# Kernel optimization log

Hardware: AMD Instinct MI355X
Metric: run time of the kernel (lower is better)

## Reference

```python
import jax, jax.numpy as jnp
import numpy as np
import math

BS, QLEN, DIM, NHEADS = 2, 2048, 1024, 16
DPH = DIM // NHEADS


def setup_inputs() -> dict:
    key = jax.random.key(0)
    ks = jax.random.split(key, 10)
    s = 0.02
    return {
        "input": jax.random.normal(ks[0], (BS, QLEN, DIM), jnp.float32),
        "mask": jax.random.randint(ks[1], (BS, QLEN), 0, 2, jnp.int32),
        "Wq": jax.random.normal(ks[2], (DIM, DIM), jnp.float32) * s,
        "bq": jnp.zeros((DIM,), jnp.float32),
        "Wk": jax.random.normal(ks[3], (DIM, DIM), jnp.float32) * s,
        "bk": jnp.zeros((DIM,), jnp.float32),
        "Wv": jax.random.normal(ks[4], (DIM, DIM), jnp.float32) * s,
        "bv": jnp.zeros((DIM,), jnp.float32),
        "Wo": jax.random.normal(ks[5], (DIM, DIM), jnp.float32) * s,
        "bo": jnp.zeros((DIM,), jnp.float32),
    }


def _shape(x):
    # (bs, len, dim) -> (bs, heads, len, dph)
    return x.reshape(BS, -1, NHEADS, DPH).transpose(0, 2, 1, 3)


def reference(input, mask, Wq, bq, Wk, bk, Wv, bv, Wo, bo):
    q = _shape(input @ Wq.T + bq)
    k = _shape(input @ Wk.T + bk)
    v = _shape(input @ Wv.T + bv)
    q = q / math.sqrt(DPH)
    scores = jnp.einsum("bhqd,bhkd->bhqk", q, k)  # (bs, h, qlen, klen)
    # original masked_fill_ with 1e-10 (NOT -inf)
    m = (mask == 0)[:, None, None, :]  # (bs,1,1,klen)
    scores = jnp.where(m, jnp.float32(1e-10), scores)
    weights = jax.nn.softmax(scores.astype(jnp.float32), axis=-1).astype(scores.dtype)
    # dropout p=0.0 / eval mode -> identity
    context = jnp.einsum("bhqk,bhkd->bhqd", weights, v)
    context = context.transpose(0, 2, 1, 3).reshape(BS, -1, DIM)
    return context @ Wo.T + bo
```

## Files before the change

kernel.cpp:

```cpp
#include <hip/hip_runtime.h>

typedef __attribute__((ext_vector_type(8))) _Float16 half8;
typedef __attribute__((ext_vector_type(4))) _Float16 half4;
typedef __attribute__((ext_vector_type(4))) float f32x4;
typedef __attribute__((ext_vector_type(16))) float f32x16;
typedef __attribute__((ext_vector_type(4))) int int4v;

#define BS 2
#define QLEN 2048
#define DIM 1024
#define NH 16
#define DPH 64
#define MTOT (BS * QLEN)
#define LOG2E 1.44269504088896340736f

__global__ void cvt_f32_f16(const float* __restrict__ src,
                            _Float16* __restrict__ dst, int n4) {
    int i = blockIdx.x * blockDim.x + threadIdx.x;
    int stride = gridDim.x * blockDim.x;
    for (int idx = i; idx < n4; idx += stride) {
        float4 v = ((const float4*)src)[idx];
        half4 o;
        o[0] = (_Float16)v.x; o[1] = (_Float16)v.y;
        o[2] = (_Float16)v.z; o[3] = (_Float16)v.w;
        ((half4*)dst)[idx] = o;
    }
}

__global__ void cvt_w4(const float* __restrict__ w0, const float* __restrict__ w1,
                       const float* __restrict__ w2, const float* __restrict__ w3,
                       _Float16* __restrict__ d0, _Float16* __restrict__ d1,
                       _Float16* __restrict__ d2, _Float16* __restrict__ d3) {
    const float* src = (blockIdx.y == 0) ? w0 : (blockIdx.y == 1) ? w1
                     : (blockIdx.y == 2) ? w2 : w3;
    _Float16* dst = (blockIdx.y == 0) ? d0 : (blockIdx.y == 1) ? d1
                  : (blockIdx.y == 2) ? d2 : d3;
    int idx = blockIdx.x * blockDim.x + threadIdx.x;
    float4 v = ((const float4*)src)[idx];
    half4 o;
    o[0] = (_Float16)v.x; o[1] = (_Float16)v.y;
    o[2] = (_Float16)v.z; o[3] = (_Float16)v.w;
    ((half4*)dst)[idx] = o;
}

__device__ __forceinline__ void gload_lds16(const _Float16* g, _Float16* l) {
    __builtin_amdgcn_global_load_lds(
        (const __attribute__((address_space(1))) void*)g,
        (__attribute__((address_space(3))) void*)l, 16, 0, 0);
}

__global__ __launch_bounds__(256) void gemm_qkv(
    const _Float16* __restrict__ A,
    const _Float16* __restrict__ Wq, const _Float16* __restrict__ Wk,
    const _Float16* __restrict__ Wv,
    const float* __restrict__ bq, const float* __restrict__ bk,
    const float* __restrict__ bv, const int* __restrict__ mask,
    _Float16* __restrict__ Qd, _Float16* __restrict__ Kd,
    _Float16* __restrict__ Vd) {
    const int K = 1024;
    __shared__ _Float16 sA[2][128 * 32];
    __shared__ _Float16 sB[2][128 * 32];
    const int z = blockIdx.z;
    const _Float16* W = (z == 0) ? Wq : (z == 1) ? Wk : Wv;
    const float* bias = (z == 0) ? bq : (z == 1) ? bk : bv;
    const int m0 = blockIdx.y * 128, n0 = blockIdx.x * 128;
    const int tid = threadIdx.x, w = tid >> 6, l = tid & 63;
    const int wr = (w >> 1) * 64, wc = (w & 1) * 64;
    const int r = l & 15, g = l >> 4;

    auto stage = [&](int k0, int bb) {
#pragma unroll
        for (int i = 0; i < 2; ++i) {
            int c = tid + i * 256;
            int row = c >> 2, seg = (c & 3) * 8;
            gload_lds16(&A[(size_t)(m0 + row) * K + k0 + seg], &sA[bb][c * 8]);
            gload_lds16(&W[(size_t)(n0 + row) * K + k0 + seg], &sB[bb][c * 8]);
        }
    };

    f32x4 acc[4][4] = {};

    stage(0, 0);
    __syncthreads();
    int buf = 0;
    for (int k0 = 0; k0 < K; k0 += 32) {
        if (k0 + 32 < K) stage(k0 + 32, buf ^ 1);

        half8 af[4], bf[4];
#pragma unroll
        for (int i = 0; i < 4; ++i) {
            af[i] = *(const half8*)&sA[buf][(wr + i * 16 + r) * 32 + g * 8];
            bf[i] = *(const half8*)&sB[buf][(wc + i * 16 + r) * 32 + g * 8];
        }
#pragma unroll
        for (int i = 0; i < 4; ++i)
#pragma unroll
            for (int j = 0; j < 4; ++j)
                acc[i][j] = __builtin_amdgcn_mfma_f32_16x16x32_f16(
                    af[i], bf[j], acc[i][j], 0, 0, 0);
        __syncthreads();
        buf ^= 1;
    }

    float bv4[4];
#pragma unroll
    for (int j = 0; j < 4; ++j) bv4[j] = bias[n0 + wc + j * 16 + r];

#pragma unroll
    for (int i = 0; i < 4; ++i)
#pragma unroll
        for (int j = 0; j < 4; ++j) {
            const int n = n0 + wc + j * 16 + r;
            const int h = n >> 6, d = n & 63;
#pragma unroll
            for (int reg = 0; reg < 4; ++reg) {
                const int m = m0 + wr + i * 16 + g * 4 + reg;
                const int bb = m >> 11, tt = m & 2047;
                float v = acc[i][j][reg] + bv4[j];
                if (z == 0)
                    Qd[(((size_t)(bb * NH + h)) * QLEN + tt) * DPH + d] =
                        (_Float16)(v * (0.125f * LOG2E));
                else if (z == 1) {
                    v = mask[bb * QLEN + tt] ? v : 0.f;
                    Kd[(((size_t)(bb * NH + h)) * QLEN + tt) * DPH + d] = (_Float16)v;
                } else
                    Vd[(((size_t)(bb * NH + h)) * DPH + d) * QLEN + tt] = (_Float16)v;
            }
        }
}

__global__ __launch_bounds__(256) void gemm_out(
    const _Float16* __restrict__ A, const _Float16* __restrict__ W,
    const float* __restrict__ bias, float* __restrict__ out) {
    const int K = 1024;
    __shared__ _Float16 sA[2][128 * 32];
    __shared__ _Float16 sB[2][128 * 32];
    const int m0 = blockIdx.y * 128, n0 = blockIdx.x * 128;
    const int tid = threadIdx.x, w = tid >> 6, l = tid & 63;
    const int wr = (w >> 1) * 64, wc = (w & 1) * 64;
    const int r = l & 15, g = l >> 4;

    auto stage = [&](int k0, int bb) {
#pragma unroll
        for (int i = 0; i < 2; ++i) {
            int c = tid + i * 256;
            int row = c >> 2, seg = (c & 3) * 8;
            gload_lds16(&A[(size_t)(m0 + row) * K + k0 + seg], &sA[bb][c * 8]);
            gload_lds16(&W[(size_t)(n0 + row) * K + k0 + seg], &sB[bb][c * 8]);
        }
    };

    f32x4 acc[4][4] = {};

    stage(0, 0);
    __syncthreads();
    int buf = 0;
    for (int k0 = 0; k0 < K; k0 += 32) {
        if (k0 + 32 < K) stage(k0 + 32, buf ^ 1);

        half8 af[4], bf[4];
#pragma unroll
        for (int i = 0; i < 4; ++i) {
            af[i] = *(const half8*)&sA[buf][(wr + i * 16 + r) * 32 + g * 8];
            bf[i] = *(const half8*)&sB[buf][(wc + i * 16 + r) * 32 + g * 8];
        }
#pragma unroll
        for (int i = 0; i < 4; ++i)
#pragma unroll
            for (int j = 0; j < 4; ++j)
                acc[i][j] = __builtin_amdgcn_mfma_f32_16x16x32_f16(
                    af[i], bf[j], acc[i][j], 0, 0, 0);
        __syncthreads();
        buf ^= 1;
    }

    float bv4[4];
#pragma unroll
    for (int j = 0; j < 4; ++j) bv4[j] = bias[n0 + wc + j * 16 + r];
#pragma unroll
    for (int i = 0; i < 4; ++i)
#pragma unroll
        for (int j = 0; j < 4; ++j) {
            const int n = n0 + wc + j * 16 + r;
#pragma unroll
            for (int reg = 0; reg < 4; ++reg) {
                const int m = m0 + wr + i * 16 + g * 4 + reg;
                out[(size_t)m * DIM + n] = acc[i][j][reg] + bv4[j];
            }
        }
}

__global__ __launch_bounds__(512) void attn_kernel(
    const _Float16* __restrict__ Qg, const _Float16* __restrict__ Kg,
    const _Float16* __restrict__ Vg, _Float16* __restrict__ ctx) {
    __shared__ __align__(16) char smem[65536];

    const int flat = blockIdx.x;
    const int qt = (flat >> 3) & 15;
    const int bh = ((flat >> 7) << 3) | (flat & 7);
    const int b = bh >> 4, h = bh & 15;
    const _Float16* __restrict__ Qp = Qg + (size_t)bh * QLEN * DPH;
    const _Float16* __restrict__ Kp = Kg + (size_t)bh * QLEN * DPH;
    const _Float16* __restrict__ Vp = Vg + (size_t)bh * DPH * QLEN;

    const int tid = threadIdx.x, w = tid >> 6, l = tid & 63;
    const int qsub = w & 3, ksplit = w >> 2;
    const int ln = l & 31, hi = l >> 5;
    const int q0 = qt * 128 + qsub * 32;
    const int kbase = ksplit * 1024;

    _Float16* sK[2];
    _Float16* sV[2];
#pragma unroll
    for (int bb = 0; bb < 2; ++bb) {
        sK[bb] = (_Float16*)(smem + (ksplit * 2 + bb) * 8192);
        sV[bb] = (_Float16*)(smem + 32768 + (ksplit * 2 + bb) * 8192);
    }

    half8 qf[4];
#pragma unroll
    for (int ks = 0; ks < 4; ++ks)
        qf[ks] = *(const half8*)&Qp[(size_t)(q0 + ln) * DPH + ks * 16 + hi * 8];

    f32x16 accT[2] = {};
    float lsum = 0.f;

    auto stage = [&](int tt, int bb) {
        const int k0 = kbase + tt * 64;
        const int c8 = ((l & 7) ^ (l >> 3)) * 8;
        const int rl = l >> 3;
#pragma unroll
        for (int j = 0; j < 2; ++j) {
            const int r0 = qsub * 16 + j * 8;
            gload_lds16(&Kp[(size_t)(k0 + r0 + rl) * DPH + c8],
                        sK[bb] + r0 * 64 + l * 8);
            gload_lds16(&Vp[(size_t)(r0 + rl) * QLEN + k0 + c8],
                        sV[bb] + r0 * 64 + l * 8);
        }
    };

    auto compute = [&](int bb) {
        const _Float16* pK = sK[bb];
        const _Float16* pV = sV[bb];
#pragma unroll
        for (int kb = 0; kb < 2; ++kb) {
            f32x16 st = {};
            __builtin_amdgcn_s_setprio(1);
#pragma unroll
            for (int ks = 0; ks < 4; ++ks) {
                const int pos = ((ks * 2 + hi) ^ (ln & 7)) * 8;
                half8 kf = *(const half8*)(pK + (kb * 32 + ln) * 64 + pos);
                st = __builtin_amdgcn_mfma_f32_32x32x16_f16(kf, qf[ks], st, 0, 0, 0);
            }
            __builtin_amdgcn_s_setprio(0);

            int cpk[8];
#pragma unroll
            for (int i = 0; i < 8; ++i) {
                float e0 = __builtin_amdgcn_exp2f(st[2 * i]);
                float e1 = __builtin_amdgcn_exp2f(st[2 * i + 1]);
                lsum += e0 + e1;
                cpk[i] =
                    __builtin_bit_cast(int, __builtin_amdgcn_cvt_pkrtz(e0, e1));
            }
            asm("v_permlane32_swap_b32 %0, %1" : "+v"(cpk[0]), "+v"(cpk[2]));
            asm("v_permlane32_swap_b32 %0, %1" : "+v"(cpk[1]), "+v"(cpk[3]));
            asm("v_permlane32_swap_b32 %0, %1" : "+v"(cpk[4]), "+v"(cpk[6]));
            asm("v_permlane32_swap_b32 %0, %1" : "+v"(cpk[5]), "+v"(cpk[7]));
            int4v b0 = {cpk[0], cpk[1], cpk[2], cpk[3]};
            int4v b1 = {cpk[4], cpk[5], cpk[6], cpk[7]};
            half8 Bf0 = __builtin_bit_cast(half8, b0);
            half8 Bf1 = __builtin_bit_cast(half8, b1);

            __builtin_amdgcn_s_setprio(1);
#pragma unroll
            for (int dblk = 0; dblk < 2; ++dblk) {
                const int j0 = ((kb * 4 + 0 + hi) ^ (ln & 7)) * 8;
                const int j1 = ((kb * 4 + 2 + hi) ^ (ln & 7)) * 8;
                half8 vf0 = *(const half8*)(pV + (dblk * 32 + ln) * 64 + j0);
                half8 vf1 = *(const half8*)(pV + (dblk * 32 + ln) * 64 + j1);
                accT[dblk] = __builtin_amdgcn_mfma_f32_32x32x16_f16(
                    vf0, Bf0, accT[dblk], 0, 0, 0);
                accT[dblk] = __builtin_amdgcn_mfma_f32_32x32x16_f16(
                    vf1, Bf1, accT[dblk], 0, 0, 0);
            }
            __builtin_amdgcn_s_setprio(0);
        }
    };

    stage(0, 0);
    __syncthreads();
    int buf = 0;
    for (int t = 0; t < 16; ++t) {
        stage((t + 1) & 15, buf ^ 1);
        compute(buf);
        __syncthreads();
        buf ^= 1;
    }

    lsum += __shfl_xor(lsum, 32);

    float* sRed = (float*)smem;
    if (ksplit == 1) {
        float* p = sRed + (qsub * 64 + l) * 33;
#pragma unroll
        for (int dblk = 0; dblk < 2; ++dblk)
#pragma unroll
            for (int i = 0; i < 16; ++i)
                p[dblk * 16 + i] = accT[dblk][i];
        p[32] = lsum;
    }
    __syncthreads();
    if (ksplit == 1) return;

    const float* p = sRed + (qsub * 64 + l) * 33;
#pragma unroll
    for (int dblk = 0; dblk < 2; ++dblk)
#pragma unroll
        for (int i = 0; i < 16; ++i)
            accT[dblk][i] += p[dblk * 16 + i];
    lsum += p[32];

    const float inv = 1.f / lsum;
    _Float16* cp = ctx + ((size_t)(b * QLEN) + q0 + ln) * DIM + h * DPH;
#pragma unroll
    for (int dblk = 0; dblk < 2; ++dblk)
#pragma unroll
        for (int j = 0; j < 4; ++j) {
            half4 o4;
#pragma unroll
            for (int e = 0; e < 4; ++e)
                o4[e] = (_Float16)(accT[dblk][4 * j + e] * inv);
            *(half4*)&cp[dblk * 32 + 8 * j + 4 * hi] = o4;
        }
}

extern "C" void kernel_launch(void* const* d_in, const int* in_sizes, int n_in,
                              void* d_out, int out_size, void* d_ws, size_t ws_size,
                              hipStream_t stream) {
    const float* x  = (const float*)d_in[0];
    const int* mask = (const int*)d_in[1];
    const float* Wq = (const float*)d_in[2];
    const float* bq = (const float*)d_in[3];
    const float* Wk = (const float*)d_in[4];
    const float* bk = (const float*)d_in[5];
    const float* Wv = (const float*)d_in[6];
    const float* bv = (const float*)d_in[7];
    const float* Wo = (const float*)d_in[8];
    const float* bo = (const float*)d_in[9];
    float* out = (float*)d_out;

    char* ws = (char*)d_ws;
    const size_t MB = 1u << 20;
    _Float16* X16  = (_Float16*)(ws + 0);
    _Float16* Wq16 = (_Float16*)(ws + 8 * MB);
    _Float16* Wk16 = (_Float16*)(ws + 10 * MB);
    _Float16* Wv16 = (_Float16*)(ws + 12 * MB);
    _Float16* Wo16 = (_Float16*)(ws + 14 * MB);
    _Float16* Q16  = (_Float16*)(ws + 16 * MB);
    _Float16* K16  = (_Float16*)(ws + 24 * MB);
    _Float16* V16T = (_Float16*)(ws + 32 * MB);
    _Float16* CTX  = (_Float16*)(ws + 40 * MB);

    cvt_f32_f16<<<2048, 256, 0, stream>>>(x, X16, MTOT * DIM / 4);
    cvt_w4<<<dim3(1024, 4), 256, 0, stream>>>(Wq, Wk, Wv, Wo,
                                              Wq16, Wk16, Wv16, Wo16);

    gemm_qkv<<<dim3(8, 32, 3), 256, 0, stream>>>(
        X16, Wq16, Wk16, Wv16, bq, bk, bv, mask, Q16, K16, V16T);

    attn_kernel<<<512, 512, 0, stream>>>(Q16, K16, V16T, CTX);

    gemm_out<<<dim3(8, 32), 256, 0, stream>>>(CTX, Wo16, bo, out);
}
```

Baseline: 142.4 us.

## Merge conversion kernels, halve out-GEMM M tile, precompute attention LDS pointers

The two fp32-to-fp16 conversion kernels become one grid-stride kernel, which removes a launch. The output projection GEMM now uses 64-row M tiles, doubling its grid to 512 blocks so more CUs are busy, at the cost of less B-tile reuse per block. The attention kernel precomputes swizzled LDS read addresses and advancing global pointers, and unrolls the double-buffer loop by two so buffer offsets are constants, which cuts per-iteration address arithmetic. The precomputed pointers may raise register pressure.

New measurement: 121.7 us. -14.5%, faster.

```diff
diff --git a/kernel.cpp b/kernel.cpp
--- a/kernel.cpp
+++ b/kernel.cpp
@@ -14,33 +14,31 @@
 #define MTOT (BS * QLEN)
 #define LOG2E 1.44269504088896340736f
 
-__global__ void cvt_f32_f16(const float* __restrict__ src,
-                            _Float16* __restrict__ dst, int n4) {
-    int i = blockIdx.x * blockDim.x + threadIdx.x;
+__global__ void cvt_all(const float* __restrict__ x,
+                        const float* __restrict__ wq, const float* __restrict__ wk,
+                        const float* __restrict__ wv, const float* __restrict__ wo,
+                        _Float16* __restrict__ X16,
+                        _Float16* __restrict__ Wq16, _Float16* __restrict__ Wk16,
+                        _Float16* __restrict__ Wv16, _Float16* __restrict__ Wo16) {
+    const int NX = (MTOT * DIM) / 4;
+    const int NW = (DIM * DIM) / 4;
+    const int total = NX + 4 * NW;
+    int idx = blockIdx.x * blockDim.x + threadIdx.x;
     int stride = gridDim.x * blockDim.x;
-    for (int idx = i; idx < n4; idx += stride) {
-        float4 v = ((const float4*)src)[idx];
+    for (int i = idx; i < total; i += stride) {
+        const float* src; _Float16* dst; int off;
+        if (i < NX) { src = x; dst = X16; off = i; }
+        else {
+            int k = i - NX; int which = k / NW; off = k - which * NW;
+            src = which == 0 ? wq : which == 1 ? wk : which == 2 ? wv : wo;
+            dst = which == 0 ? Wq16 : which == 1 ? Wk16 : which == 2 ? Wv16 : Wo16;
+        }
+        float4 v = ((const float4*)src)[off];
         half4 o;
         o[0] = (_Float16)v.x; o[1] = (_Float16)v.y;
         o[2] = (_Float16)v.z; o[3] = (_Float16)v.w;
-        ((half4*)dst)[idx] = o;
-    }
-}
-
-__global__ void cvt_w4(const float* __restrict__ w0, const float* __restrict__ w1,
-                       const float* __restrict__ w2, const float* __restrict__ w3,
-                       _Float16* __restrict__ d0, _Float16* __restrict__ d1,
-                       _Float16* __restrict__ d2, _Float16* __restrict__ d3) {
-    const float* src = (blockIdx.y == 0) ? w0 : (blockIdx.y == 1) ? w1
-                     : (blockIdx.y == 2) ? w2 : w3;
-    _Float16* dst = (blockIdx.y == 0) ? d0 : (blockIdx.y == 1) ? d1
-                  : (blockIdx.y == 2) ? d2 : d3;
-    int idx = blockIdx.x * blockDim.x + threadIdx.x;
-    float4 v = ((const float4*)src)[idx];
-    half4 o;
-    o[0] = (_Float16)v.x; o[1] = (_Float16)v.y;
-    o[2] = (_Float16)v.z; o[3] = (_Float16)v.w;
-    ((half4*)dst)[idx] = o;
+        ((half4*)dst)[off] = o;
+    }
 }
 
 __device__ __forceinline__ void gload_lds16(const _Float16* g, _Float16* l) {
@@ -133,24 +131,28 @@
     const _Float16* __restrict__ A, const _Float16* __restrict__ W,
     const float* __restrict__ bias, float* __restrict__ out) {
     const int K = 1024;
-    __shared__ _Float16 sA[2][128 * 32];
+    __shared__ _Float16 sA[2][64 * 32];
     __shared__ _Float16 sB[2][128 * 32];
-    const int m0 = blockIdx.y * 128, n0 = blockIdx.x * 128;
+    const int m0 = blockIdx.y * 64, n0 = blockIdx.x * 128;
     const int tid = threadIdx.x, w = tid >> 6, l = tid & 63;
-    const int wr = (w >> 1) * 64, wc = (w & 1) * 64;
+    const int wr = (w >> 1) * 32, wc = (w & 1) * 64;
     const int r = l & 15, g = l >> 4;
 
     auto stage = [&](int k0, int bb) {
+        {
+            int c = tid;
+            int row = c >> 2, seg = (c & 3) * 8;
+            gload_lds16(&A[(size_t)(m0 + row) * K + k0 + seg], &sA[bb][c * 8]);
+        }
 #pragma unroll
         for (int i = 0; i < 2; ++i) {
             int c = tid + i * 256;
             int row = c >> 2, seg = (c & 3) * 8;
-            gload_lds16(&A[(size_t)(m0 + row) * K + k0 + seg], &sA[bb][c * 8]);
             gload_lds16(&W[(size_t)(n0 + row) * K + k0 + seg], &sB[bb][c * 8]);
         }
     };
 
-    f32x4 acc[4][4] = {};
+    f32x4 acc[2][4] = {};
 
     stage(0, 0);
     __syncthreads();
@@ -158,14 +160,15 @@
     for (int k0 = 0; k0 < K; k0 += 32) {
         if (k0 + 32 < K) stage(k0 + 32, buf ^ 1);
 
-        half8 af[4], bf[4];
-#pragma unroll
-        for (int i = 0; i < 4; ++i) {
+        half8 af[2], bf[4];
+#pragma unroll
+        for (int i = 0; i < 2; ++i)
             af[i] = *(const half8*)&sA[buf][(wr + i * 16 + r) * 32 + g * 8];
-            bf[i] = *(const half8*)&sB[buf][(wc + i * 16 + r) * 32 + g * 8];
-        }
-#pragma unroll
-        for (int i = 0; i < 4; ++i)
+#pragma unroll
+        for (int j = 0; j < 4; ++j)
+            bf[j] = *(const half8*)&sB[buf][(wc + j * 16 + r) * 32 + g * 8];
+#pragma unroll
+        for (int i = 0; i < 2; ++i)
 #pragma unroll
             for (int j = 0; j < 4; ++j)
                 acc[i][j] = __builtin_amdgcn_mfma_f32_16x16x32_f16(
@@ -178,7 +181,7 @@
 #pragma unroll
     for (int j = 0; j < 4; ++j) bv4[j] = bias[n0 + wc + j * 16 + r];
 #pragma unroll
-    for (int i = 0; i < 4; ++i)
+    for (int i = 0; i < 2; ++i)
 #pragma unroll
         for (int j = 0; j < 4; ++j) {
             const int n = n0 + wc + j * 16 + r;
@@ -209,13 +212,8 @@
     const int q0 = qt * 128 + qsub * 32;
     const int kbase = ksplit * 1024;
 
-    _Float16* sK[2];
-    _Float16* sV[2];
-#pragma unroll
-    for (int bb = 0; bb < 2; ++bb) {
-        sK[bb] = (_Float16*)(smem + (ksplit * 2 + bb) * 8192);
-        sV[bb] = (_Float16*)(smem + 32768 + (ksplit * 2 + bb) * 8192);
-    }
+    _Float16* sK0 = (_Float16*)(smem + ksplit * 2 * 8192);
+    _Float16* sV0 = (_Float16*)(smem + 32768 + ksplit * 2 * 8192);
 
     half8 qf[4];
 #pragma unroll
@@ -225,31 +223,56 @@
     f32x16 accT[2] = {};
     float lsum = 0.f;
 
-    auto stage = [&](int tt, int bb) {
-        const int k0 = kbase + tt * 64;
-        const int c8 = ((l & 7) ^ (l >> 3)) * 8;
-        const int rl = l >> 3;
+    const _Float16* kptr[2][4];
+    const _Float16* vptr[2][2][2];
+#pragma unroll
+    for (int kb = 0; kb < 2; ++kb) {
+#pragma unroll
+        for (int ks = 0; ks < 4; ++ks)
+            kptr[kb][ks] = sK0 + (kb * 32 + ln) * 64 + ((ks * 2 + hi) ^ (ln & 7)) * 8;
+#pragma unroll
+        for (int dblk = 0; dblk < 2; ++dblk) {
+            vptr[kb][dblk][0] =
+                sV0 + (dblk * 32 + ln) * 64 + ((kb * 4 + 0 + hi) ^ (ln & 7)) * 8;
+            vptr[kb][dblk][1] =
+                sV0 + (dblk * 32 + ln) * 64 + ((kb * 4 + 2 + hi) ^ (ln & 7)) * 8;
+        }
+    }
+
+    const int c8 = ((l & 7) ^ (l >> 3)) * 8;
+    const int rl = l >> 3;
+    const _Float16* gK[2];
+    const _Float16* gV[2];
+    _Float16* dK[2];
+    _Float16* dV[2];
+#pragma unroll
+    for (int j = 0; j < 2; ++j) {
+        const int r0 = qsub * 16 + j * 8;
+        gK[j] = &Kp[(size_t)(kbase + r0 + rl) * DPH + c8];
+        gV[j] = &Vp[(size_t)(r0 + rl) * QLEN + kbase + c8];
+        dK[j] = sK0 + r0 * 64 + l * 8;
+        dV[j] = sV0 + r0 * 64 + l * 8;
+    }
+
+    auto stageAdv = [&](int bb) {
 #pragma unroll
         for (int j = 0; j < 2; ++j) {
-            const int r0 = qsub * 16 + j * 8;
-            gload_lds16(&Kp[(size_t)(k0 + r0 + rl) * DPH + c8],
-                        sK[bb] + r0 * 64 + l * 8);
-            gload_lds16(&Vp[(size_t)(r0 + rl) * QLEN + k0 + c8],
-                        sV[bb] + r0 * 64 + l * 8);
+            gload_lds16(gK[j], dK[j] + bb * 4096);
+            gload_lds16(gV[j], dV[j] + bb * 4096);
+            gK[j] += 64 * DPH;
+            gV[j] += 64;
         }
     };
 
     auto compute = [&](int bb) {
-        const _Float16* pK = sK[bb];
-        const _Float16* pV = sV[bb];
+        const int boff = bb * 4096;
 #pragma unroll
         for (int kb = 0; kb < 2; ++kb) {
             f32x16 st = {};
             __builtin_amdgcn_s_setprio(1);
 #pragma unroll
             for (int ks = 0; ks < 4; ++ks) {
-                const int pos = ((ks * 2 + hi) ^ (ln & 7)) * 8;
-                half8 kf = *(const half8*)(pK + (kb * 32 + ln) * 64 + pos);
+                half8 kf = *(const half8*)(kptr[kb][ks] + boff);
                 st = __builtin_amdgcn_mfma_f32_32x32x16_f16(kf, qf[ks], st, 0, 0, 0);
             }
             __builtin_amdgcn_s_setprio(0);
@@ -275,10 +298,8 @@
             __builtin_amdgcn_s_setprio(1);
 #pragma unroll
             for (int dblk = 0; dblk < 2; ++dblk) {
-                const int j0 = ((kb * 4 + 0 + hi) ^ (ln & 7)) * 8;
-                const int j1 = ((kb * 4 + 2 + hi) ^ (ln & 7)) * 8;
-                half8 vf0 = *(const half8*)(pV + (dblk * 32 + ln) * 64 + j0);
-                half8 vf1 = *(const half8*)(pV + (dblk * 32 + ln) * 64 + j1);
+                half8 vf0 = *(const half8*)(vptr[kb][dblk][0] + boff);
+                half8 vf1 = *(const half8*)(vptr[kb][dblk][1] + boff);
                 accT[dblk] = __builtin_amdgcn_mfma_f32_32x32x16_f16(
                     vf0, Bf0, accT[dblk], 0, 0, 0);
                 accT[dblk] = __builtin_amdgcn_mfma_f32_32x32x16_f16(
@@ -288,14 +309,15 @@
         }
     };
 
-    stage(0, 0);
+    stageAdv(0);
     __syncthreads();
-    int buf = 0;
-    for (int t = 0; t < 16; ++t) {
-        stage((t + 1) & 15, buf ^ 1);
-        compute(buf);
+    for (int t = 0; t < 8; ++t) {
+        stageAdv(1);
+        compute(0);
         __syncthreads();
-        buf ^= 1;
+        stageAdv(0);
+        compute(1);
+        __syncthreads();
     }
 
     lsum += __shfl_xor(lsum, 32);
@@ -362,14 +384,13 @@
     _Float16* V16T = (_Float16*)(ws + 32 * MB);
     _Float16* CTX  = (_Float16*)(ws + 40 * MB);
 
-    cvt_f32_f16<<<2048, 256, 0, stream>>>(x, X16, MTOT * DIM / 4);
-    cvt_w4<<<dim3(1024, 4), 256, 0, stream>>>(Wq, Wk, Wv, Wo,
-                                              Wq16, Wk16, Wv16, Wo16);
+    cvt_all<<<2048, 256, 0, stream>>>(x, Wq, Wk, Wv, Wo,
+                                      X16, Wq16, Wk16, Wv16, Wo16);
 
     gemm_qkv<<<dim3(8, 32, 3), 256, 0, stream>>>(
         X16, Wq16, Wk16, Wv16, bq, bk, bv, mask, Q16, K16, V16T);
 
     attn_kernel<<<512, 512, 0, stream>>>(Q16, K16, V16T, CTX);
 
-    gemm_out<<<dim3(8, 32), 256, 0, stream>>>(CTX, Wo16, bo, out);
-}
+    gemm_out<<<dim3(8, 64), 256, 0, stream>>>(CTX, Wo16, bo, out);
+}
```
